# Optimization experiments

Measured on AMD Instinct MI355X. Metric: run time of the kernel, lower is better.

The kernel has to match this reference:

```python
import jax, jax.numpy as jnp
import numpy as np

NUM_ROUTING = 3

def squash(s):
    # squash along the unit_size axis (axis=2), exactly as the torch module
    mag_sq = jnp.sum(s * s, axis=2, keepdims=True)
    mag = jnp.sqrt(mag_sq)
    return mag_sq / (1.0 + mag_sq) * (s / mag)

def setup_inputs() -> dict:
    key = jax.random.key(0)
    k1, k2 = jax.random.split(key)
    B, in_unit, in_channel = 512, 8, 1152
    num_unit, unit_size = 10, 16
    x = jax.random.normal(k1, (B, in_unit, in_channel), dtype=jnp.float32)
    weight = jax.random.normal(k2, (in_channel, num_unit, unit_size, in_unit), dtype=jnp.float32)
    return {"x": x, "weight": weight}

def reference(x, weight):
    B = x.shape[0]
    C, J = weight.shape[0], weight.shape[1]  # in_channel, num_unit
    xt = jnp.swapaxes(x, 1, 2)  # [B, C, in_unit]
    # u_hat[c, j, b, s] = W[c, j, s, :] @ x[b, c, :]
    u_hat = jnp.einsum('cjsi,bci->cjbs', weight, xt)  # [C, J, B, S]
    b_ij = jnp.zeros((C, J), dtype=x.dtype)
    v = None
    for _ in range(NUM_ROUTING):
        # DGL degree-bucketing puts all J capsule nodes in one bucket, so the
        # softmax(dim=0) in capsule_reduce is over the num_unit axis per input capsule
        c = jax.nn.softmax(b_ij, axis=1)          # [C, J]
        s = jnp.einsum('cj,cjbs->jbs', c, u_hat)  # [J, B, S]
        v = squash(s)                             # [J, B, S]
        # update_edge: b_ij += mean over batch of <v_j, u_hat_ij>
        b_ij = b_ij + jnp.einsum('jbs,cjbs->cj', v, u_hat) / B
    # [J, B, S] -> [B, J, S] -> unsqueeze(1).unsqueeze(4).squeeze(1) -> [B, J, S, 1]
    return jnp.transpose(v, (1, 0, 2))[..., None]
```

## Files before the change

### kernel.cpp

```cpp
#include <hip/hip_runtime.h>
#include <hip/hip_bf16.h>
#include <math.h>

#define B_  512
#define I_  8
#define C_  1152
#define J_  10
#define S_  16
#define K1  9216
#define NKB 288
#define KBT 16

typedef short short8 __attribute__((ext_vector_type(8)));
typedef float floatx4 __attribute__((ext_vector_type(4)));

__device__ inline unsigned short f2bf(float f) {
    unsigned int u = __float_as_uint(f);
    return (unsigned short)((u + 0x7FFFu + ((u >> 16) & 1u)) >> 16);
}
__device__ inline unsigned int pack2(float a, float b) {
    __hip_bfloat162 h = __float22bfloat162_rn(float2{a, b});
    return *reinterpret_cast<unsigned int*>(&h);
}

__global__ __launch_bounds__(512) void k_pack(const float* __restrict__ x,
                                              const float* __restrict__ W,
                                              uint4* __restrict__ Bs,
                                              uint4* __restrict__ Bt,
                                              uint4* __restrict__ Wf,
                                              unsigned short* __restrict__ W2,
                                              float* __restrict__ b_ij) {
    __shared__ float lds[10240];
    const int task = blockIdx.x;
    const int t = threadIdx.x;
    const int w = t >> 6, L = t & 63, quad = L >> 4;

    if (task < 576) {
        const int bt = task / 36, kt = task % 36;
        const int b0 = bt * 32, k0 = kt * 256;
        #pragma unroll
        for (int p = 0; p < 4; p++) {
            int f4 = p * 512 + t;
            int row = f4 >> 6, c4 = (f4 & 63) << 2;
            *(float4*)&lds[row * 260 + c4] =
                *(const float4*)&x[(size_t)(b0 + row) * K1 + k0 + c4];
        }
        __syncthreads();
        #pragma unroll
        for (int p = 0; p < 2; p++) {
            const int bl = p * 16 + (L & 15);
            const float* s = &lds[bl * 260 + w * 32 + quad * 8];
            uint4 o;
            o.x = pack2(s[0], s[1]); o.y = pack2(s[2], s[3]);
            o.z = pack2(s[4], s[5]); o.w = pack2(s[6], s[7]);
            Bs[((size_t)(bt * 2 + p) * NKB + kt * 8 + w) * 64 + L] = o;
        }
        #pragma unroll
        for (int p = 0; p < 2; p++) {
            const int ntl = w * 2 + p;
            const int nl = ntl * 16 + (L & 15);
            float v[8];
            #pragma unroll
            for (int e = 0; e < 8; e++) v[e] = lds[(quad * 8 + e) * 260 + nl];
            uint4 o;
            o.x = pack2(v[0], v[1]); o.y = pack2(v[2], v[3]);
            o.z = pack2(v[4], v[5]); o.w = pack2(v[6], v[7]);
            Bt[((size_t)(kt * 16 + ntl) * KBT + bt) * 64 + L] = o;
        }
    } else if (task < 720) {
        const int c0 = (task - 576) * 8;
        #pragma unroll
        for (int p = 0; p < 5; p++) {
            int f4 = p * 512 + t;
            int cc = f4 / 320, off4 = (f4 % 320) << 2;
            *(float4*)&lds[cc * 1280 + off4] =
                *(const float4*)&W[(size_t)(c0 + cc) * 1280 + off4];
        }
        __syncthreads();
        #pragma unroll
        for (int p = 0; p < 3; p++) {
            int o = p * 512 + t;
            if (o < 1280) {
                int j = o >> 7, i = (o >> 4) & 7, m = o & 15;
                int k0w = i * C_ + c0;
                int Lw = m | (((k0w >> 3) & 3) << 4);
                float v[8];
                #pragma unroll
                for (int e = 0; e < 8; e++)
                    v[e] = lds[e * 1280 + j * 128 + m * 8 + i];
                uint4 og;
                og.x = pack2(v[0], v[1]); og.y = pack2(v[2], v[3]);
                og.z = pack2(v[4], v[5]); og.w = pack2(v[6], v[7]);
                Wf[((size_t)j * NKB + (k0w >> 5)) * 64 + Lw] = og;
            }
        }
        #pragma unroll
        for (int p = 0; p < 2; p++) {
            int o = p * 512 + t;
            if (o < 640) {
                int j = o >> 6, i = (o >> 3) & 7, cc = o & 7;
                unsigned int r8[8];
                #pragma unroll
                for (int h = 0; h < 8; h++)
                    r8[h] = pack2(lds[cc * 1280 + j * 128 + (2 * h) * 8 + i],
                                  lds[cc * 1280 + j * 128 + (2 * h + 1) * 8 + i]);
                unsigned short* dst = W2 + ((size_t)(j * 8 + i) * C_ + c0 + cc) * 16;
                *(uint4*)dst       = make_uint4(r8[0], r8[1], r8[2], r8[3]);
                *(uint4*)(dst + 8) = make_uint4(r8[4], r8[5], r8[6], r8[7]);
            }
        }
    } else {
        for (int idx = t; idx < C_ * J_; idx += 512) b_ij[idx] = 0.0f;
    }
}

__global__ __launch_bounds__(512) void k_sgemm_f(const short8* __restrict__ Wf,
                                                 const short8* __restrict__ Bs,
                                                 const float* __restrict__ b_ij,
                                                 unsigned short* __restrict__ Vf,
                                                 float* __restrict__ out,
                                                 int mode) {
    __shared__ float smf[1152 + 2048];
    const int t = threadIdx.x, w = t >> 6, L = t & 63, quad = L >> 4;
    const int j  = blockIdx.y;
    const int nt = blockIdx.x;

    if (mode) {
        for (int c = t; c < C_; c += 512) {
            float bv[J_], mx = -1e30f;
            #pragma unroll
            for (int jj = 0; jj < J_; jj++) {
                bv[jj] = b_ij[c * J_ + jj]; mx = fmaxf(mx, bv[jj]);
            }
            float sum = 0.0f;
            #pragma unroll
            for (int jj = 0; jj < J_; jj++) sum += __expf(bv[jj] - mx);
            smf[c] = __expf(bv[j] - mx) / sum;
        }
    }
    __syncthreads();

    const short8* pA = Wf + ((size_t)j * NKB + w * 36) * 64 + L;
    const short8* pB = Bs + ((size_t)nt * NKB + w * 36) * 64 + L;
    floatx4 acc = {0.f, 0.f, 0.f, 0.f};
    if (mode) {
        #pragma unroll 6
        for (int i = 0; i < 36; i++) {
            short8 a = pA[i * 64];
            const int cb = i * 32 + quad * 8;
            float4 cl = *(const float4*)&smf[cb];
            float4 ch = *(const float4*)&smf[cb + 4];
            float cn8[8] = {cl.x, cl.y, cl.z, cl.w, ch.x, ch.y, ch.z, ch.w};
            unsigned int* au = (unsigned int*)&a;
            short8 a2; unsigned int* ao = (unsigned int*)&a2;
            #pragma unroll
            for (int h = 0; h < 4; h++) {
                float f0 = __uint_as_float(au[h] << 16)         * cn8[2 * h];
                float f1 = __uint_as_float(au[h] & 0xffff0000u) * cn8[2 * h + 1];
                ao[h] = pack2(f0, f1);
            }
            acc = __builtin_amdgcn_mfma_f32_16x16x32_bf16(a2, pB[i * 64], acc, 0, 0, 0);
        }
    } else {
        #pragma unroll 6
        for (int i = 0; i < 36; i++)
            acc = __builtin_amdgcn_mfma_f32_16x16x32_bf16(pA[i * 64], pB[i * 64], acc, 0, 0, 0);
    }

    const int col = L & 15, rw = quad << 2;
    float* base = &smf[1152 + w * 256];
    #pragma unroll
    for (int r = 0; r < 4; r++)
        base[(rw + r) * 16 + col] = acc[r];
    __syncthreads();

    if (t < 16) {
        float sv[S_]; float msq = 0.f;
        #pragma unroll
        for (int s = 0; s < S_; s++) {
            float a = 0.f;
            #pragma unroll
            for (int w8 = 0; w8 < 8; w8++)
                a += smf[1152 + w8 * 256 + s * 16 + t];
            if (mode == 0) a *= 0.1f;
            sv[s] = a; msq += a * a;
        }
        const float scale = msq / ((1.f + msq) * sqrtf(msq));
        const int b = nt * 16 + t;
        if (mode < 2) {
            const int kb = b >> 5, lh = (b >> 3) & 3, e = b & 7;
            #pragma unroll
            for (int s = 0; s < S_; s++)
                Vf[((size_t)(j * KBT + kb) * 64 + (s | (lh << 4))) * 8 + e] =
                    f2bf(sv[s] * scale);
        } else {
            float o16[S_];
            #pragma unroll
            for (int s = 0; s < S_; s++) o16[s] = sv[s] * scale;
            float* dst = &out[((size_t)b * J_ + j) * S_];
            #pragma unroll
            for (int r4 = 0; r4 < 4; r4++)
                *(float4*)(dst + r4 * 4) = *(float4*)(o16 + r4 * 4);
        }
    }
}

__global__ __launch_bounds__(512) void k_tgemm_bup(const short8* __restrict__ Vf,
                                                   const short8* __restrict__ Bt,
                                                   const unsigned short* __restrict__ W2,
                                                   float* __restrict__ b_ij) {
    const int t = threadIdx.x, w = t >> 6, L = t & 63;
    const int j = blockIdx.y, ntg = blockIdx.x;
    const int nt = ntg * 8 + w;
    const short8* pA = Vf + (size_t)j * KBT * 64 + L;
    const short8* pB = Bt + (size_t)nt * KBT * 64 + L;
    floatx4 a = {0.f, 0.f, 0.f, 0.f};
    #pragma unroll
    for (int kb = 0; kb < KBT; kb++)
        a = __builtin_amdgcn_mfma_f32_16x16x32_bf16(pA[kb * 64], pB[kb * 64], a, 0, 0, 0);
    const int col = L & 15, rw = (L >> 4) << 2;
    const int i = nt / 72;
    const int c = (nt % 72) * 16 + col;
    const unsigned short* wp = W2 + ((size_t)(j * 8 + i) * C_ + c) * 16 + rw;
    uint2 wv = *(const uint2*)wp;
    float p = a[0] * __uint_as_float((unsigned int)wv.x << 16)
            + a[1] * __uint_as_float(wv.x & 0xffff0000u)
            + a[2] * __uint_as_float((unsigned int)wv.y << 16)
            + a[3] * __uint_as_float(wv.y & 0xffff0000u);
    p += __shfl_xor(p, 16);
    p += __shfl_xor(p, 32);
    if ((L >> 4) == 0)
        atomicAdd(&b_ij[c * J_ + j], p * (1.0f / 512.f));
}

extern "C" void kernel_launch(void* const* d_in, const int* in_sizes, int n_in,
                              void* d_out, int out_size, void* d_ws, size_t ws_size,
                              hipStream_t stream) {
    const float* x = (const float*)d_in[0];
    const float* W = (const float*)d_in[1];
    float* out = (float*)d_out;
    float* ws  = (float*)d_ws;

    float* Bs_f = ws;
    float* Bt_f = Bs_f + 2359296;
    float* Wf_f = Bt_f + 2359296;
    float* W2_f = Wf_f + 737280;
    float* Vf_f = W2_f + 737280;
    float* bij  = Vf_f + 40960;

    k_pack<<<721, 512, 0, stream>>>(x, W, (uint4*)Bs_f, (uint4*)Bt_f,
                                    (uint4*)Wf_f, (unsigned short*)W2_f, bij);

    k_sgemm_f<<<dim3(32, 10), 512, 0, stream>>>(
        (const short8*)Wf_f, (const short8*)Bs_f, bij,
        (unsigned short*)Vf_f, out, 0);
    k_tgemm_bup<<<dim3(72, 10), 512, 0, stream>>>(
        (const short8*)Vf_f, (const short8*)Bt_f, (const unsigned short*)W2_f, bij);

    k_sgemm_f<<<dim3(32, 10), 512, 0, stream>>>(
        (const short8*)Wf_f, (const short8*)Bs_f, bij,
        (unsigned short*)Vf_f, out, 1);
    k_tgemm_bup<<<dim3(72, 10), 512, 0, stream>>>(
        (const short8*)Vf_f, (const short8*)Bt_f, (const unsigned short*)W2_f, bij);

    k_sgemm_f<<<dim3(32, 10), 512, 0, stream>>>(
        (const short8*)Wf_f, (const short8*)Bs_f, bij,
        (unsigned short*)Vf_f, out, 2);
}
```

Measured before the change: 134.1 us.

## Fuse all routing phases into one persistent kernel with grid barriers

Replaces the six separate launches (pack, three sgemm, two tgemm) with a single persistent kernel of 320 blocks. The phases are separated by an atomic-counter grid barrier, and the counter is reset with a memset on each launch. This removes the per-launch overhead and the inter-kernel gaps. In exchange it depends on all 320 blocks being co-resident and adds spin-wait barrier costs. The tgemm and pack work is now distributed with grid-stride loops.

```diff
diff --git a/kernel.cpp b/kernel.cpp
--- a/kernel.cpp
+++ b/kernel.cpp
@@ -2,14 +2,15 @@
 #include <hip/hip_bf16.h>
 #include <math.h>
 
-#define B_  512
-#define I_  8
-#define C_  1152
-#define J_  10
-#define S_  16
-#define K1  9216
-#define NKB 288
-#define KBT 16
+#define B_   512
+#define I_   8
+#define C_   1152
+#define J_   10
+#define S_   16
+#define K1   9216
+#define NKB  288
+#define KBT  16
+#define NBLK 320
 
 typedef short short8 __attribute__((ext_vector_type(8)));
 typedef float floatx4 __attribute__((ext_vector_type(4)));
@@ -23,109 +24,28 @@
     return *reinterpret_cast<unsigned int*>(&h);
 }
 
-__global__ __launch_bounds__(512) void k_pack(const float* __restrict__ x,
-                                              const float* __restrict__ W,
-                                              uint4* __restrict__ Bs,
-                                              uint4* __restrict__ Bt,
-                                              uint4* __restrict__ Wf,
-                                              unsigned short* __restrict__ W2,
-                                              float* __restrict__ b_ij) {
-    __shared__ float lds[10240];
-    const int task = blockIdx.x;
-    const int t = threadIdx.x;
-    const int w = t >> 6, L = t & 63, quad = L >> 4;
-
-    if (task < 576) {
-        const int bt = task / 36, kt = task % 36;
-        const int b0 = bt * 32, k0 = kt * 256;
-        #pragma unroll
-        for (int p = 0; p < 4; p++) {
-            int f4 = p * 512 + t;
-            int row = f4 >> 6, c4 = (f4 & 63) << 2;
-            *(float4*)&lds[row * 260 + c4] =
-                *(const float4*)&x[(size_t)(b0 + row) * K1 + k0 + c4];
-        }
-        __syncthreads();
-        #pragma unroll
-        for (int p = 0; p < 2; p++) {
-            const int bl = p * 16 + (L & 15);
-            const float* s = &lds[bl * 260 + w * 32 + quad * 8];
-            uint4 o;
-            o.x = pack2(s[0], s[1]); o.y = pack2(s[2], s[3]);
-            o.z = pack2(s[4], s[5]); o.w = pack2(s[6], s[7]);
-            Bs[((size_t)(bt * 2 + p) * NKB + kt * 8 + w) * 64 + L] = o;
-        }
-        #pragma unroll
-        for (int p = 0; p < 2; p++) {
-            const int ntl = w * 2 + p;
-            const int nl = ntl * 16 + (L & 15);
-            float v[8];
-            #pragma unroll
-            for (int e = 0; e < 8; e++) v[e] = lds[(quad * 8 + e) * 260 + nl];
-            uint4 o;
-            o.x = pack2(v[0], v[1]); o.y = pack2(v[2], v[3]);
-            o.z = pack2(v[4], v[5]); o.w = pack2(v[6], v[7]);
-            Bt[((size_t)(kt * 16 + ntl) * KBT + bt) * 64 + L] = o;
-        }
-    } else if (task < 720) {
-        const int c0 = (task - 576) * 8;
-        #pragma unroll
-        for (int p = 0; p < 5; p++) {
-            int f4 = p * 512 + t;
-            int cc = f4 / 320, off4 = (f4 % 320) << 2;
-            *(float4*)&lds[cc * 1280 + off4] =
-                *(const float4*)&W[(size_t)(c0 + cc) * 1280 + off4];
-        }
-        __syncthreads();
-        #pragma unroll
-        for (int p = 0; p < 3; p++) {
-            int o = p * 512 + t;
-            if (o < 1280) {
-                int j = o >> 7, i = (o >> 4) & 7, m = o & 15;
-                int k0w = i * C_ + c0;
-                int Lw = m | (((k0w >> 3) & 3) << 4);
-                float v[8];
-                #pragma unroll
-                for (int e = 0; e < 8; e++)
-                    v[e] = lds[e * 1280 + j * 128 + m * 8 + i];
-                uint4 og;
-                og.x = pack2(v[0], v[1]); og.y = pack2(v[2], v[3]);
-                og.z = pack2(v[4], v[5]); og.w = pack2(v[6], v[7]);
-                Wf[((size_t)j * NKB + (k0w >> 5)) * 64 + Lw] = og;
-            }
-        }
-        #pragma unroll
-        for (int p = 0; p < 2; p++) {
-            int o = p * 512 + t;
-            if (o < 640) {
-                int j = o >> 6, i = (o >> 3) & 7, cc = o & 7;
-                unsigned int r8[8];
-                #pragma unroll
-                for (int h = 0; h < 8; h++)
-                    r8[h] = pack2(lds[cc * 1280 + j * 128 + (2 * h) * 8 + i],
-                                  lds[cc * 1280 + j * 128 + (2 * h + 1) * 8 + i]);
-                unsigned short* dst = W2 + ((size_t)(j * 8 + i) * C_ + c0 + cc) * 16;
-                *(uint4*)dst       = make_uint4(r8[0], r8[1], r8[2], r8[3]);
-                *(uint4*)(dst + 8) = make_uint4(r8[4], r8[5], r8[6], r8[7]);
-            }
-        }
-    } else {
-        for (int idx = t; idx < C_ * J_; idx += 512) b_ij[idx] = 0.0f;
-    }
-}
-
-__global__ __launch_bounds__(512) void k_sgemm_f(const short8* __restrict__ Wf,
-                                                 const short8* __restrict__ Bs,
-                                                 const float* __restrict__ b_ij,
-                                                 unsigned short* __restrict__ Vf,
-                                                 float* __restrict__ out,
-                                                 int mode) {
-    __shared__ float smf[1152 + 2048];
+__device__ inline void gsync(int* bar, int target) {
+    __syncthreads();
+    if (threadIdx.x == 0) {
+        __threadfence();
+        __hip_atomic_fetch_add(bar, 1, __ATOMIC_RELEASE, __HIP_MEMORY_SCOPE_AGENT);
+        while (__hip_atomic_load(bar, __ATOMIC_ACQUIRE, __HIP_MEMORY_SCOPE_AGENT) < target)
+            __builtin_amdgcn_s_sleep(2);
+    }
+    __syncthreads();
+}
+
+template<int MODE>
+__device__ __forceinline__ void sgemm_phase(
+        float* smf,
+        const short8* __restrict__ Wf, const short8* __restrict__ Bs,
+        const float* __restrict__ b_ij,
+        unsigned short* __restrict__ Vf, float* __restrict__ out) {
     const int t = threadIdx.x, w = t >> 6, L = t & 63, quad = L >> 4;
-    const int j  = blockIdx.y;
-    const int nt = blockIdx.x;
-
-    if (mode) {
+    const int j  = blockIdx.x >> 5;
+    const int nt = blockIdx.x & 31;
+
+    if (MODE) {
         for (int c = t; c < C_; c += 512) {
             float bv[J_], mx = -1e30f;
             #pragma unroll
@@ -143,7 +63,7 @@
     const short8* pA = Wf + ((size_t)j * NKB + w * 36) * 64 + L;
     const short8* pB = Bs + ((size_t)nt * NKB + w * 36) * 64 + L;
     floatx4 acc = {0.f, 0.f, 0.f, 0.f};
-    if (mode) {
+    if (MODE) {
         #pragma unroll 6
         for (int i = 0; i < 36; i++) {
             short8 a = pA[i * 64];
@@ -182,12 +102,12 @@
             #pragma unroll
             for (int w8 = 0; w8 < 8; w8++)
                 a += smf[1152 + w8 * 256 + s * 16 + t];
-            if (mode == 0) a *= 0.1f;
+            if (MODE == 0) a *= 0.1f;
             sv[s] = a; msq += a * a;
         }
         const float scale = msq / ((1.f + msq) * sqrtf(msq));
         const int b = nt * 16 + t;
-        if (mode < 2) {
+        if (MODE < 2) {
             const int kb = b >> 5, lh = (b >> 3) & 3, e = b & 7;
             #pragma unroll
             for (int s = 0; s < S_; s++)
@@ -205,32 +125,146 @@
     }
 }
 
-__global__ __launch_bounds__(512) void k_tgemm_bup(const short8* __restrict__ Vf,
-                                                   const short8* __restrict__ Bt,
-                                                   const unsigned short* __restrict__ W2,
-                                                   float* __restrict__ b_ij) {
+__device__ __forceinline__ void tgemm_phase(
+        const short8* __restrict__ Vf, const short8* __restrict__ Bt,
+        const unsigned short* __restrict__ W2, float* __restrict__ b_ij) {
     const int t = threadIdx.x, w = t >> 6, L = t & 63;
-    const int j = blockIdx.y, ntg = blockIdx.x;
-    const int nt = ntg * 8 + w;
-    const short8* pA = Vf + (size_t)j * KBT * 64 + L;
-    const short8* pB = Bt + (size_t)nt * KBT * 64 + L;
-    floatx4 a = {0.f, 0.f, 0.f, 0.f};
-    #pragma unroll
-    for (int kb = 0; kb < KBT; kb++)
-        a = __builtin_amdgcn_mfma_f32_16x16x32_bf16(pA[kb * 64], pB[kb * 64], a, 0, 0, 0);
-    const int col = L & 15, rw = (L >> 4) << 2;
-    const int i = nt / 72;
-    const int c = (nt % 72) * 16 + col;
-    const unsigned short* wp = W2 + ((size_t)(j * 8 + i) * C_ + c) * 16 + rw;
-    uint2 wv = *(const uint2*)wp;
-    float p = a[0] * __uint_as_float((unsigned int)wv.x << 16)
-            + a[1] * __uint_as_float(wv.x & 0xffff0000u)
-            + a[2] * __uint_as_float((unsigned int)wv.y << 16)
-            + a[3] * __uint_as_float(wv.y & 0xffff0000u);
-    p += __shfl_xor(p, 16);
-    p += __shfl_xor(p, 32);
-    if ((L >> 4) == 0)
-        atomicAdd(&b_ij[c * J_ + j], p * (1.0f / 512.f));
+    for (int tau = blockIdx.x * 8 + w; tau < 5760; tau += NBLK * 8) {
+        const int j = tau / 576, nt = tau % 576;
+        const short8* pA = Vf + (size_t)j * KBT * 64 + L;
+        const short8* pB = Bt + (size_t)nt * KBT * 64 + L;
+        floatx4 a = {0.f, 0.f, 0.f, 0.f};
+        #pragma unroll
+        for (int kb = 0; kb < KBT; kb++)
+            a = __builtin_amdgcn_mfma_f32_16x16x32_bf16(pA[kb * 64], pB[kb * 64], a, 0, 0, 0);
+        const int col = L & 15, rw = (L >> 4) << 2;
+        const int i = nt / 72;
+        const int c = (nt % 72) * 16 + col;
+        const unsigned short* wp = W2 + ((size_t)(j * 8 + i) * C_ + c) * 16 + rw;
+        uint2 wv = *(const uint2*)wp;
+        float p = a[0] * __uint_as_float((unsigned int)wv.x << 16)
+                + a[1] * __uint_as_float(wv.x & 0xffff0000u)
+                + a[2] * __uint_as_float((unsigned int)wv.y << 16)
+                + a[3] * __uint_as_float(wv.y & 0xffff0000u);
+        p += __shfl_xor(p, 16);
+        p += __shfl_xor(p, 32);
+        if ((L >> 4) == 0)
+            atomicAdd(&b_ij[c * J_ + j], p * (1.0f / 512.f));
+    }
+}
+
+__global__ __launch_bounds__(512, 4) void k_fused(
+        const float* __restrict__ x, const float* __restrict__ W,
+        float* __restrict__ ws, float* __restrict__ out, int* __restrict__ bar) {
+    __shared__ float lds[10240];
+    const int t = threadIdx.x, w = t >> 6, L = t & 63, quad = L >> 4;
+
+    float* Bs_f = ws;
+    float* Bt_f = Bs_f + 2359296;
+    float* Wf_f = Bt_f + 2359296;
+    float* W2_f = Wf_f + 737280;
+    float* Vf_f = W2_f + 737280;
+    float* bij  = Vf_f + 40960;
+
+    uint4* Bs4 = (uint4*)Bs_f;
+    uint4* Bt4 = (uint4*)Bt_f;
+    uint4* Wf4 = (uint4*)Wf_f;
+    unsigned short* W2s = (unsigned short*)W2_f;
+
+    for (int task = blockIdx.x; task < 721; task += NBLK) {
+        if (task < 576) {
+            const int bt = task / 36, kt = task % 36;
+            const int b0 = bt * 32, k0 = kt * 256;
+            #pragma unroll
+            for (int p = 0; p < 4; p++) {
+                int f4 = p * 512 + t;
+                int row = f4 >> 6, c4 = (f4 & 63) << 2;
+                *(float4*)&lds[row * 260 + c4] =
+                    *(const float4*)&x[(size_t)(b0 + row) * K1 + k0 + c4];
+            }
+            __syncthreads();
+            #pragma unroll
+            for (int p = 0; p < 2; p++) {
+                const int bl = p * 16 + (L & 15);
+                const float* s = &lds[bl * 260 + w * 32 + quad * 8];
+                uint4 o;
+                o.x = pack2(s[0], s[1]); o.y = pack2(s[2], s[3]);
+                o.z = pack2(s[4], s[5]); o.w = pack2(s[6], s[7]);
+                Bs4[((size_t)(bt * 2 + p) * NKB + kt * 8 + w) * 64 + L] = o;
+            }
+            #pragma unroll
+            for (int p = 0; p < 2; p++) {
+                const int ntl = w * 2 + p;
+                const int nl = ntl * 16 + (L & 15);
+                float v[8];
+                #pragma unroll
+                for (int e = 0; e < 8; e++) v[e] = lds[(quad * 8 + e) * 260 + nl];
+                uint4 o;
+                o.x = pack2(v[0], v[1]); o.y = pack2(v[2], v[3]);
+                o.z = pack2(v[4], v[5]); o.w = pack2(v[6], v[7]);
+                Bt4[((size_t)(kt * 16 + ntl) * KBT + bt) * 64 + L] = o;
+            }
+        } else if (task < 720) {
+            const int c0 = (task - 576) * 8;
+            #pragma unroll
+            for (int p = 0; p < 5; p++) {
+                int f4 = p * 512 + t;
+                int cc = f4 / 320, off4 = (f4 % 320) << 2;
+                *(float4*)&lds[cc * 1280 + off4] =
+                    *(const float4*)&W[(size_t)(c0 + cc) * 1280 + off4];
+            }
+            __syncthreads();
+            #pragma unroll
+            for (int p = 0; p < 3; p++) {
+                int o = p * 512 + t;
+                if (o < 1280) {
+                    int j = o >> 7, i = (o >> 4) & 7, m = o & 15;
+                    int k0w = i * C_ + c0;
+                    int Lw = m | (((k0w >> 3) & 3) << 4);
+                    float v[8];
+                    #pragma unroll
+                    for (int e = 0; e < 8; e++)
+                        v[e] = lds[e * 1280 + j * 128 + m * 8 + i];
+                    uint4 og;
+                    og.x = pack2(v[0], v[1]); og.y = pack2(v[2], v[3]);
+                    og.z = pack2(v[4], v[5]); og.w = pack2(v[6], v[7]);
+                    Wf4[((size_t)j * NKB + (k0w >> 5)) * 64 + Lw] = og;
+                }
+            }
+            #pragma unroll
+            for (int p = 0; p < 2; p++) {
+                int o = p * 512 + t;
+                if (o < 640) {
+                    int j = o >> 6, i = (o >> 3) & 7, cc = o & 7;
+                    unsigned int r8[8];
+                    #pragma unroll
+                    for (int h = 0; h < 8; h++)
+                        r8[h] = pack2(lds[cc * 1280 + j * 128 + (2 * h) * 8 + i],
+                                      lds[cc * 1280 + j * 128 + (2 * h + 1) * 8 + i]);
+                    unsigned short* dst = W2s + ((size_t)(j * 8 + i) * C_ + c0 + cc) * 16;
+                    *(uint4*)dst       = make_uint4(r8[0], r8[1], r8[2], r8[3]);
+                    *(uint4*)(dst + 8) = make_uint4(r8[4], r8[5], r8[6], r8[7]);
+                }
+            }
+        } else {
+            for (int idx = t; idx < C_ * J_; idx += 512) bij[idx] = 0.0f;
+        }
+        __syncthreads();
+    }
+
+    gsync(bar, 1 * NBLK);
+    sgemm_phase<0>(lds, (const short8*)Wf_f, (const short8*)Bs_f, bij,
+                   (unsigned short*)Vf_f, out);
+    gsync(bar, 2 * NBLK);
+    tgemm_phase((const short8*)Vf_f, (const short8*)Bt_f, W2s, bij);
+    gsync(bar, 3 * NBLK);
+    sgemm_phase<1>(lds, (const short8*)Wf_f, (const short8*)Bs_f, bij,
+                   (unsigned short*)Vf_f, out);
+    gsync(bar, 4 * NBLK);
+    tgemm_phase((const short8*)Vf_f, (const short8*)Bt_f, W2s, bij);
+    gsync(bar, 5 * NBLK);
+    sgemm_phase<2>(lds, (const short8*)Wf_f, (const short8*)Bs_f, bij,
+                   (unsigned short*)Vf_f, out);
 }
 
 extern "C" void kernel_launch(void* const* d_in, const int* in_sizes, int n_in,
@@ -241,29 +275,8 @@
     float* out = (float*)d_out;
     float* ws  = (float*)d_ws;
 
-    float* Bs_f = ws;
-    float* Bt_f = Bs_f + 2359296;
-    float* Wf_f = Bt_f + 2359296;
-    float* W2_f = Wf_f + 737280;
-    float* Vf_f = W2_f + 737280;
-    float* bij  = Vf_f + 40960;
-
-    k_pack<<<721, 512, 0, stream>>>(x, W, (uint4*)Bs_f, (uint4*)Bt_f,
-                                    (uint4*)Wf_f, (unsigned short*)W2_f, bij);
-
-    k_sgemm_f<<<dim3(32, 10), 512, 0, stream>>>(
-        (const short8*)Wf_f, (const short8*)Bs_f, bij,
-        (unsigned short*)Vf_f, out, 0);
-    k_tgemm_bup<<<dim3(72, 10), 512, 0, stream>>>(
-        (const short8*)Vf_f, (const short8*)Bt_f, (const unsigned short*)W2_f, bij);
-
-    k_sgemm_f<<<dim3(32, 10), 512, 0, stream>>>(
-        (const short8*)Wf_f, (const short8*)Bs_f, bij,
-        (unsigned short*)Vf_f, out, 1);
-    k_tgemm_bup<<<dim3(72, 10), 512, 0, stream>>>(
-        (const short8*)Vf_f, (const short8*)Bt_f, (const unsigned short*)W2_f, bij);
-
-    k_sgemm_f<<<dim3(32, 10), 512, 0, stream>>>(
-        (const short8*)Wf_f, (const short8*)Bs_f, bij,
-        (unsigned short*)Vf_f, out, 2);
-}
+    int* bar = (int*)(ws + 2359296 * 2 + 737280 * 2 + 40960 + 11520);
+    hipMemsetAsync(bar, 0, 256, stream);
+
+    k_fused<<<NBLK, 512, 0, stream>>>(x, W, ws, out, bar);
+}
```

Measured after the change: 453.2 us. +238.0%, slower.

## Remap blocks to XCDs for L2 locality and drop atomics in b_ij update

Applied to the files above, without the earlier changes.

Both GEMM kernels now run on a 1D grid whose block indices are remapped so that blocks landing on the same XCD (bid&7) share j or c ranges, with the aim of improving L2 reuse of W and B tiles. In the transpose GEMM, each block now holds all 8 in_unit slices for one 16-channel block, so the 8 waves reduce through shared memory and one thread per column does a single plain add to b_ij in place of per-wave global atomics. This depends on no other block touching the same b_ij entries, which holds because each (cblk, j) pair belongs to exactly one block. It adds a __syncthreads.

```diff
diff --git a/kernel.cpp b/kernel.cpp
--- a/kernel.cpp
+++ b/kernel.cpp
@@ -122,8 +122,10 @@
                                                  int mode) {
     __shared__ float smf[1152 + 2048];
     const int t = threadIdx.x, w = t >> 6, L = t & 63, quad = L >> 4;
-    const int j  = blockIdx.y;
-    const int nt = blockIdx.x;
+    const int bid = blockIdx.x;
+    const int xcd = bid & 7, sl = bid >> 3;
+    const int j  = 5 * (xcd >> 2) + sl % 5;
+    const int nt = 8 * (xcd & 3) + sl / 5;
 
     if (mode) {
         for (int c = t; c < C_; c += 512) {
@@ -209,9 +211,13 @@
                                                    const short8* __restrict__ Bt,
                                                    const unsigned short* __restrict__ W2,
                                                    float* __restrict__ b_ij) {
+    __shared__ float red[8][16];
     const int t = threadIdx.x, w = t >> 6, L = t & 63;
-    const int j = blockIdx.y, ntg = blockIdx.x;
-    const int nt = ntg * 8 + w;
+    const int bid = blockIdx.x;
+    const int xcd = bid & 7, sl = bid >> 3;
+    const int cblk = 9 * xcd + sl / 10;
+    const int j    = sl % 10;
+    const int nt   = w * 72 + cblk;
     const short8* pA = Vf + (size_t)j * KBT * 64 + L;
     const short8* pB = Bt + (size_t)nt * KBT * 64 + L;
     floatx4 a = {0.f, 0.f, 0.f, 0.f};
@@ -219,9 +225,8 @@
     for (int kb = 0; kb < KBT; kb++)
         a = __builtin_amdgcn_mfma_f32_16x16x32_bf16(pA[kb * 64], pB[kb * 64], a, 0, 0, 0);
     const int col = L & 15, rw = (L >> 4) << 2;
-    const int i = nt / 72;
-    const int c = (nt % 72) * 16 + col;
-    const unsigned short* wp = W2 + ((size_t)(j * 8 + i) * C_ + c) * 16 + rw;
+    const int c = cblk * 16 + col;
+    const unsigned short* wp = W2 + ((size_t)(j * 8 + w) * C_ + c) * 16 + rw;
     uint2 wv = *(const uint2*)wp;
     float p = a[0] * __uint_as_float((unsigned int)wv.x << 16)
             + a[1] * __uint_as_float(wv.x & 0xffff0000u)
@@ -229,8 +234,15 @@
             + a[3] * __uint_as_float(wv.y & 0xffff0000u);
     p += __shfl_xor(p, 16);
     p += __shfl_xor(p, 32);
-    if ((L >> 4) == 0)
-        atomicAdd(&b_ij[c * J_ + j], p * (1.0f / 512.f));
+    if ((L >> 4) == 0) red[w][col] = p;
+    __syncthreads();
+    if (t < 16) {
+        float acc = 0.f;
+        #pragma unroll
+        for (int w8 = 0; w8 < 8; w8++) acc += red[w8][t];
+        const size_t idx = (size_t)(cblk * 16 + t) * J_ + j;
+        b_ij[idx] += acc * (1.0f / 512.f);
+    }
 }
 
 extern "C" void kernel_launch(void* const* d_in, const int* in_sizes, int n_in,
@@ -251,19 +263,19 @@
     k_pack<<<721, 512, 0, stream>>>(x, W, (uint4*)Bs_f, (uint4*)Bt_f,
                                     (uint4*)Wf_f, (unsigned short*)W2_f, bij);
 
-    k_sgemm_f<<<dim3(32, 10), 512, 0, stream>>>(
+    k_sgemm_f<<<320, 512, 0, stream>>>(
         (const short8*)Wf_f, (const short8*)Bs_f, bij,
         (unsigned short*)Vf_f, out, 0);
-    k_tgemm_bup<<<dim3(72, 10), 512, 0, stream>>>(
+    k_tgemm_bup<<<720, 512, 0, stream>>>(
         (const short8*)Vf_f, (const short8*)Bt_f, (const unsigned short*)W2_f, bij);
 
-    k_sgemm_f<<<dim3(32, 10), 512, 0, stream>>>(
+    k_sgemm_f<<<320, 512, 0, stream>>>(
         (const short8*)Wf_f, (const short8*)Bs_f, bij,
         (unsigned short*)Vf_f, out, 1);
-    k_tgemm_bup<<<dim3(72, 10), 512, 0, stream>>>(
+    k_tgemm_bup<<<720, 512, 0, stream>>>(
         (const short8*)Vf_f, (const short8*)Bt_f, (const unsigned short*)W2_f, bij);
 
-    k_sgemm_f<<<dim3(32, 10), 512, 0, stream>>>(
+    k_sgemm_f<<<320, 512, 0, stream>>>(
         (const short8*)Wf_f, (const short8*)Bs_f, bij,
         (unsigned short*)Vf_f, out, 2);
 }
```

Result: faster. 129.9 us (-3.1%).
